# Kernel optimization log

Hardware: AMD Instinct MI355X
Metric: run time of the kernel (lower is better)

The kernel has to match this reference:

```python
import jax, jax.numpy as jnp
import numpy as np

B, T, D = 256, 256, 96   # batch, seq (== block_size), d_model
H, E = 6, 16             # n_head, d_head = d_model // n_head
DFF = 4 * D              # feedforward hidden = 384
NOISE_STD = 0.1
EPS = 1e-5               # torch LayerNorm default eps


def setup_inputs() -> dict:
    key = jax.random.key(0)
    ks = jax.random.split(key, 10)
    s = 0.02
    return {
        "x":     jax.random.normal(ks[0], (B, T, D), jnp.float32),
        # per-head Q/K/V projections stacked: [H, D, E] (no bias, as in Head)
        "Wq":    jax.random.normal(ks[1], (H, D, E), jnp.float32) * s,
        "Wk":    jax.random.normal(ks[2], (H, D, E), jnp.float32) * s,
        "Wv":    jax.random.normal(ks[3], (H, D, E), jnp.float32) * s,
        "Wp":    jax.random.normal(ks[4], (D, D), jnp.float32) * s,
        "bp":    jnp.zeros((D,), jnp.float32),
        "ln1_g": jnp.ones((D,), jnp.float32),
        "ln1_b": jnp.zeros((D,), jnp.float32),
        "ln2_g": jnp.ones((D,), jnp.float32),
        "ln2_b": jnp.zeros((D,), jnp.float32),
        "W1":    jax.random.normal(ks[5], (D, DFF), jnp.float32) * s,
        "b1":    jnp.zeros((DFF,), jnp.float32),
        "W2":    jax.random.normal(ks[6], (DFF, D), jnp.float32) * s,
        "b2":    jnp.zeros((D,), jnp.float32),
    }


def layernorm(x, g, b):
    m = jnp.mean(x, axis=-1, keepdims=True)
    v = jnp.var(x, axis=-1, keepdims=True)
    return (x - m) * jax.lax.rsqrt(v + EPS) * g + b


def reference(x, Wq, Wk, Wv, Wp, bp, ln1_g, ln1_b, ln2_g, ln2_b, W1, b1, W2, b2):
    Bx, Tx, Dx = x.shape
    nk1, nk2 = jax.random.split(jax.random.key(42), 2)

    # --- self-attention branch (pre-norm) ---
    h = layernorm(x, ln1_g, ln1_b)
    q = jnp.einsum('btd,hde->bhte', h, Wq)
    k = jnp.einsum('btd,hde->bhte', h, Wk)
    v = jnp.einsum('btd,hde->bhte', h, Wv)
    scores = jnp.einsum('bhte,bhse->bhts', q, k) * (E ** -0.5)
    causal = jnp.tril(jnp.ones((Tx, Tx), bool))
    scores = jnp.where(causal, scores, -jnp.inf)
    a = jax.nn.softmax(scores, axis=-1)      # dropout = identity (eval)
    o = jnp.einsum('bhts,bhse->bhte', a, v)
    o = o.transpose(0, 2, 1, 3).reshape(Bx, Tx, Dx)  # concat heads
    o = o @ Wp + bp
    x = x + o + jax.random.normal(nk1, x.shape, x.dtype) * NOISE_STD

    # --- feedforward branch (pre-norm) ---
    h = layernorm(x, ln2_g, ln2_b)
    f = jax.nn.relu(h @ W1 + b1) @ W2 + b2   # dropout = identity (eval)
    x = x + f + jax.random.normal(nk2, x.shape, x.dtype) * NOISE_STD
    return x
```

## Files before the change

kernel.cpp:

```cpp
#include <hip/hip_runtime.h>
#include <hip/hip_bf16.h>
#include <stdint.h>


#define B_    256
#define T_    256
#define D_    96
#define H_    6
#define E_    16
#define DFF_  384
#define BT_   (B_*T_)
#define NTOK_ (BT_*D_)
#define WPN_  (96*96)
#define W1N_  (96*384)
#define W2N_  (384*96)
#define WTOT_ (WPN_+W1N_+W2N_)

typedef __hip_bfloat16 bf16;
typedef __attribute__((ext_vector_type(8))) short v8s;
typedef __attribute__((ext_vector_type(4))) float v4f;

__device__ __forceinline__ void wfence(){ __asm__ volatile("" ::: "memory"); }

__host__ __device__ inline uint32_t rotl32(uint32_t x, int r){ return (x<<r)|(x>>(32-r)); }

__host__ __device__ inline void tf2x32(uint32_t k0, uint32_t k1, uint32_t& x0, uint32_t& x1){
  uint32_t ks2 = k0 ^ k1 ^ 0x1BD11BDAu;
  x0 += k0; x1 += k1;
#define TF_R(r) { x0 += x1; x1 = rotl32(x1, r); x1 ^= x0; }
  TF_R(13) TF_R(15) TF_R(26) TF_R(6)
  x0 += k1;  x1 += ks2 + 1u;
  TF_R(17) TF_R(29) TF_R(16) TF_R(24)
  x0 += ks2; x1 += k0 + 2u;
  TF_R(13) TF_R(15) TF_R(26) TF_R(6)
  x0 += k0;  x1 += k1 + 3u;
  TF_R(17) TF_R(29) TF_R(16) TF_R(24)
  x0 += k1;  x1 += ks2 + 4u;
  TF_R(13) TF_R(15) TF_R(26) TF_R(6)
  x0 += ks2; x1 += k0 + 5u;
#undef TF_R
}

__device__ __forceinline__ float erfinv32(float x){
  float w = -0.69314718056f * __log2f((1.0f - x) * (1.0f + x));
  float p;
  if (w < 5.0f) {
    w -= 2.5f;
    p = 2.81022636e-08f;
    p = fmaf(p, w, 3.43273939e-07f);
    p = fmaf(p, w, -3.5233877e-06f);
    p = fmaf(p, w, -4.39150654e-06f);
    p = fmaf(p, w, 0.00021858087f);
    p = fmaf(p, w, -0.00125372503f);
    p = fmaf(p, w, -0.00417768164f);
    p = fmaf(p, w, 0.246640727f);
    p = fmaf(p, w, 1.50140941f);
  } else {
    w = sqrtf(w) - 3.0f;
    p = -0.000200214257f;
    p = fmaf(p, w, 0.000100950558f);
    p = fmaf(p, w, 0.00134934322f);
    p = fmaf(p, w, -0.00367342844f);
    p = fmaf(p, w, 0.00573950773f);
    p = fmaf(p, w, -0.0076224613f);
    p = fmaf(p, w, 0.00943887047f);
    p = fmaf(p, w, 1.00167406f);
    p = fmaf(p, w, 2.83297682f);
  }
  return p * x;
}

__device__ __forceinline__ float jax_normal(uint32_t k0, uint32_t k1, uint32_t j){
  uint32_t x0 = 0u, x1 = j;
  tf2x32(k0, k1, x0, x1);
  uint32_t bits = x0 ^ x1;
  float f = __uint_as_float((bits >> 9) | 0x3F800000u) - 1.0f;
  const float lo = -0.99999994f;
  float u = fmaxf(lo, fmaf(f, 2.0f, lo));
  return 1.41421356f * erfinv32(u);
}

__device__ __forceinline__ float blo(uint32_t u){ return __uint_as_float(u << 16); }
__device__ __forceinline__ float bhi(uint32_t u){ return __uint_as_float(u & 0xFFFF0000u); }
__device__ __forceinline__ uint16_t f2b(float f){
  union { bf16 h; uint16_t u; } x; x.h = __float2bfloat16(f); return x.u;
}
__device__ __forceinline__ uint32_t packbf(float a, float b){
  return (uint32_t)f2b(a) | ((uint32_t)f2b(b) << 16);
}

__global__ __launch_bounds__(256, 3)
void k_attn_fused(const float* __restrict__ x,
                  const float* __restrict__ Wq, const float* __restrict__ Wk,
                  const float* __restrict__ Wv,
                  const float* __restrict__ g1, const float* __restrict__ bln1,
                  bf16* __restrict__ o_ws,
                  const float* __restrict__ Wp, const float* __restrict__ W1,
                  const float* __restrict__ W2, bf16* __restrict__ wbuf)
{
  __shared__ __align__(16) uint16_t hts[64*104];
  __shared__ __align__(16) uint32_t wpl[48][52];
  __shared__ __align__(16) uint16_t Ks[256][24];
  __shared__ __align__(16) uint16_t Vt[16][264];

  const int tid  = threadIdx.x;
  const int bh   = blockIdx.x;
  const int b    = bh / H_, h = bh % H_;
  const int w    = tid >> 6;
  const int lane = tid & 63;
  const int quad = lane >> 4;
  const int l15  = lane & 15;

  if (tid < 54) {
    int id = bh*54 + tid;
    const float* src; bf16* dst; int k, n, N;
    if (id < WPN_)             { src = Wp; dst = wbuf;               k = id/96; n = id%96; N = 96; }
    else if (id < WPN_ + W1N_) { int t = id - WPN_;
                                 src = W1; dst = wbuf + WPN_;        k = t/384; n = t%384; N = 384; }
    else                       { int t = id - WPN_ - W1N_;
                                 src = W2; dst = wbuf + WPN_ + W1N_; k = t/96;  n = t%96;  N = 96; }
    int idx = ((k>>3)*(N>>4) + (n>>4))*128 + ((n&15)<<3) + (k&7);
    dst[idx] = __float2bfloat16(src[(size_t)k*N + n]);
  }

  for (int idx = tid; idx < 48*48; idx += 256) {
    int c = idx / 48, dp = idx % 48;
    int mat = c >> 4, e = c & 15;
    const float* Wm = (mat == 0 ? Wk : (mat == 1 ? Wv : Wq)) + h*(D_*E_);
    wpl[c][dp] = packbf(Wm[(2*dp)*16 + e], Wm[(2*dp+1)*16 + e]);
  }

  v4f qacc[4];
  {
    const int r  = lane >> 2;
    const int cg = lane & 3;
    float gv[24], bv[24];
    #pragma unroll
    for (int i = 0; i < 24; ++i) { gv[i] = g1[cg*24 + i]; bv[i] = bln1[cg*24 + i]; }

    for (int rt = 0; rt < 4; ++rt) {
      __syncthreads();
      const int lrow = w*16 + r;
      const int row  = rt*64 + lrow;
      const float4* xp = (const float4*)(x + ((size_t)(b*256 + row)*96 + cg*24));
      float xv[24];
      #pragma unroll
      for (int p = 0; p < 6; ++p) {
        float4 t4 = xp[p];
        xv[4*p+0] = t4.x; xv[4*p+1] = t4.y; xv[4*p+2] = t4.z; xv[4*p+3] = t4.w;
      }
      float s1 = 0.f, s2 = 0.f;
      #pragma unroll
      for (int i = 0; i < 24; ++i) { s1 += xv[i]; s2 = fmaf(xv[i], xv[i], s2); }
      s1 += __shfl_xor(s1, 1); s2 += __shfl_xor(s2, 1);
      s1 += __shfl_xor(s1, 2); s2 += __shfl_xor(s2, 2);
      float mm = s1 * (1.0f/96.0f);
      float rs = rsqrtf(s2 * (1.0f/96.0f) - mm*mm + 1e-5f);
      #pragma unroll
      for (int p = 0; p < 12; ++p) {
        float h0 = (xv[2*p]   - mm)*rs*gv[2*p]   + bv[2*p];
        float h1 = (xv[2*p+1] - mm)*rs*gv[2*p+1] + bv[2*p+1];
        *(uint32_t*)&hts[lrow*104 + cg*24 + 2*p] = packbf(h0, h1);
      }
      __syncthreads();

      v8s ah[3];
      #pragma unroll
      for (int ks = 0; ks < 3; ++ks)
        ah[ks] = *(const v8s*)&hts[(w*16 + l15)*104 + ks*32 + quad*8];
      #pragma unroll
      for (int nt = 0; nt < 3; ++nt) {
        v4f acc = {0.f,0.f,0.f,0.f};
        #pragma unroll
        for (int ks = 0; ks < 3; ++ks) {
          v8s bb = *(const v8s*)&wpl[nt*16 + l15][ks*16 + quad*4];
          acc = __builtin_amdgcn_mfma_f32_16x16x32_bf16(ah[ks], bb, acc, 0, 0, 0);
        }
        int tr0 = rt*64 + w*16 + quad*4;
        if (nt == 0) {
          #pragma unroll
          for (int r2 = 0; r2 < 4; ++r2) Ks[tr0 + r2][l15] = f2b(acc[r2]);
        } else if (nt == 1) {
          *(uint32_t*)&Vt[l15][tr0]     = packbf(acc[0], acc[1]);
          *(uint32_t*)&Vt[l15][tr0 + 2] = packbf(acc[2], acc[3]);
        } else {
          qacc[rt] = acc;
        }
      }
    }
  }
  __syncthreads();

  uint16_t* Pb = &hts[(w*16)*104];
  v8s qf[4];
  v8s zero8;
  #pragma unroll
  for (int j = 0; j < 8; ++j) zero8[j] = 0;
  #pragma unroll
  for (int rt = 0; rt < 4; ++rt) {
    wfence();
    #pragma unroll
    for (int r2 = 0; r2 < 4; ++r2)
      Pb[(quad*4 + r2)*40 + l15] = f2b(qacc[rt][r2] * 0.25f);
    wfence();
    qf[rt] = (quad < 2) ? *(const v8s*)&Pb[l15*40 + quad*8] : zero8;
  }

  v8s ones;
  #pragma unroll
  for (int j = 0; j < 8; ++j) ones[j] = (short)0x3F80;

  v4f oacc[4], lac[4];
  #pragma unroll
  for (int i = 0; i < 4; ++i) { oacc[i] = (v4f){0.f,0.f,0.f,0.f}; lac[i] = (v4f){0.f,0.f,0.f,0.f}; }

  for (int sb = 0; sb < 8; ++sb) {
    v8s kf0 = (quad < 2) ? *(const v8s*)&Ks[sb*32      + l15][quad*8] : zero8;
    v8s kf1 = (quad < 2) ? *(const v8s*)&Ks[sb*32 + 16 + l15][quad*8] : zero8;
    v8s vf  = *(const v8s*)&Vt[l15][sb*32 + quad*8];
    #pragma unroll
    for (int i = 0; i < 4; ++i) {
      int mt = 4*i + w;
      if (mt >= 2*sb) {
        v4f z = {0.f,0.f,0.f,0.f};
        v4f s0 = __builtin_amdgcn_mfma_f32_16x16x32_bf16(qf[i], kf0, z, 0, 0, 0);
        v4f s1 = __builtin_amdgcn_mfma_f32_16x16x32_bf16(qf[i], kf1, z, 0, 0, 0);
        const int qb  = mt*16 + quad*4;
        const int sc0 = sb*32 + l15, sc1 = sc0 + 16;
        wfence();
        #pragma unroll
        for (int r2 = 0; r2 < 4; ++r2) {
          float p0 = (sc0 > qb + r2) ? 0.f : __expf(s0[r2]);
          float p1 = (sc1 > qb + r2) ? 0.f : __expf(s1[r2]);
          Pb[(quad*4 + r2)*40 + l15]      = f2b(p0);
          Pb[(quad*4 + r2)*40 + 16 + l15] = f2b(p1);
        }
        wfence();
        v8s pf = *(const v8s*)&Pb[l15*40 + quad*8];
        oacc[i] = __builtin_amdgcn_mfma_f32_16x16x32_bf16(pf, vf,   oacc[i], 0, 0, 0);
        lac[i]  = __builtin_amdgcn_mfma_f32_16x16x32_bf16(pf, ones, lac[i],  0, 0, 0);
      }
    }
  }

  #pragma unroll
  for (int i = 0; i < 4; ++i) {
    int mt = 4*i + w;
    #pragma unroll
    for (int r2 = 0; r2 < 4; ++r2) {
      float inv = 1.0f / lac[i][r2];
      size_t idx = ((size_t)b*256 + mt*16 + quad*4 + r2)*96 + h*16 + l15;
      o_ws[idx] = __float2bfloat16(oacc[i][r2] * inv);
    }
  }
}

__global__ __launch_bounds__(256, 6)
void k_proj_ff(const float* __restrict__ x, const bf16* __restrict__ o_ws,
               const bf16* __restrict__ wb,
               const float* __restrict__ bp,
               const float* __restrict__ g2, const float* __restrict__ bln2,
               const float* __restrict__ b1, const float* __restrict__ b2,
               float* __restrict__ out,
               uint32_t n1k0, uint32_t n1k1, uint32_t n2k0, uint32_t n2k1)
{
  __shared__ __align__(16) uint16_t t2[2][32][104];
  __shared__ __align__(8)  float2  st[32][2];

  const bf16* wpb = wb;
  const bf16* w1b = wb + WPN_;
  const bf16* w2b = wb + WPN_ + W1N_;

  const int tid  = threadIdx.x;
  const int w    = tid >> 6;
  const int wp   = w >> 1;
  const int s    = w & 1;
  const int lane = tid & 63;
  const int quad = lane >> 4;
  const int l15  = lane & 15;
  const int rowbase = blockIdx.x * 32;
  const uint32_t jbase = (uint32_t)rowbase * 96u;
  const int rloc = wp*16 + quad*4;

  #define BFRAG(Wb, Ndiv16, nt, k8) \
    (*(const v8s*)((Wb) + (((k8)*(Ndiv16) + (nt))*128 + l15*8)))

  float ff[12];
  {
    v8s ao[3];
    #pragma unroll
    for (int ks = 0; ks < 3; ++ks)
      ao[ks] = *(const v8s*)(o_ws + (size_t)(rowbase + wp*16 + l15)*96 + ks*32 + quad*8);
    #pragma unroll
    for (int nt3 = 0; nt3 < 3; ++nt3) {
      int nt = s*3 + nt3;
      int col = nt*16 + l15;
      v4f acc = {0.f,0.f,0.f,0.f};
      #pragma unroll
      for (int ks = 0; ks < 3; ++ks)
        acc = __builtin_amdgcn_mfma_f32_16x16x32_bf16(ao[ks], BFRAG(wpb, 6, nt, ks*4+quad), acc, 0, 0, 0);
      float bpv = bp[col];
      #pragma unroll
      for (int r = 0; r < 4; ++r) {
        int row = rloc + r;
        uint32_t j = jbase + (uint32_t)row*96u + (uint32_t)col;
        ff[nt3*4+r] = acc[r] + bpv + x[j] + 0.1f * jax_normal(n1k0, n1k1, j);
      }
    }
  }

  {
    float s1p[4], s2p[4];
    #pragma unroll
    for (int r = 0; r < 4; ++r) {
      float s1 = 0.f, s2 = 0.f;
      #pragma unroll
      for (int nt3 = 0; nt3 < 3; ++nt3) { float v = ff[nt3*4+r]; s1 += v; s2 = fmaf(v, v, s2); }
      s1 += __shfl_xor(s1, 1); s2 += __shfl_xor(s2, 1);
      s1 += __shfl_xor(s1, 2); s2 += __shfl_xor(s2, 2);
      s1 += __shfl_xor(s1, 4); s2 += __shfl_xor(s2, 4);
      s1 += __shfl_xor(s1, 8); s2 += __shfl_xor(s2, 8);
      s1p[r] = s1; s2p[r] = s2;
    }
    if (l15 == 0) {
      #pragma unroll
      for (int r = 0; r < 4; ++r) st[rloc + r][s] = make_float2(s1p[r], s2p[r]);
    }
    __syncthreads();

    float g2v[3], b2l[3];
    #pragma unroll
    for (int nt3 = 0; nt3 < 3; ++nt3) {
      g2v[nt3] = g2[s*48 + nt3*16 + l15];
      b2l[nt3] = bln2[s*48 + nt3*16 + l15];
    }
    #pragma unroll
    for (int r = 0; r < 4; ++r) {
      float2 pa = st[rloc + r][0], pb = st[rloc + r][1];
      float s1 = pa.x + pb.x, s2 = pa.y + pb.y;
      float mm = s1 * (1.0f/96.0f);
      float rs = rsqrtf(s2 * (1.0f/96.0f) - mm*mm + 1e-5f);
      #pragma unroll
      for (int nt3 = 0; nt3 < 3; ++nt3)
        t2[0][rloc + r][s*48 + nt3*16 + l15] =
            f2b((ff[nt3*4+r] - mm) * rs * g2v[nt3] + b2l[nt3]);
    }
  }
  __syncthreads();

  v8s ah[3];
  #pragma unroll
  for (int ks = 0; ks < 3; ++ks)
    ah[ks] = *(const v8s*)&t2[0][wp*16 + l15][ks*32 + quad*8];
  v4f acc2[3];
  #pragma unroll
  for (int nt3 = 0; nt3 < 3; ++nt3) acc2[nt3] = (v4f){0.f,0.f,0.f,0.f};
  float n2v[12];

  #define FF1C(C, DST) { \
    _Pragma("unroll") \
    for (int nt3 = 0; nt3 < 3; ++nt3) { \
      v4f a = {0.f,0.f,0.f,0.f}; \
      _Pragma("unroll") \
      for (int ks = 0; ks < 3; ++ks) \
        a = __builtin_amdgcn_mfma_f32_16x16x32_bf16(ah[ks], BFRAG(w1b, 24, (C)*6 + s*3 + nt3, ks*4+quad), a, 0, 0, 0); \
      float b1v = b1[(C)*96 + s*48 + nt3*16 + l15]; \
      _Pragma("unroll") \
      for (int r = 0; r < 4; ++r) \
        DST[rloc + r][s*48 + nt3*16 + l15] = f2b(fmaxf(a[r] + b1v, 0.f)); \
    } }

  #define FF2C(C, SRC) { \
    v8s af[3]; \
    _Pragma("unroll") \
    for (int ks = 0; ks < 3; ++ks) \
      af[ks] = *(const v8s*)&SRC[wp*16 + l15][ks*32 + quad*8]; \
    _Pragma("unroll") \
    for (int nt3 = 0; nt3 < 3; ++nt3) { \
      _Pragma("unroll") \
      for (int ks = 0; ks < 3; ++ks) \
        acc2[nt3] = __builtin_amdgcn_mfma_f32_16x16x32_bf16(af[ks], BFRAG(w2b, 6, s*3 + nt3, ((C)*3+ks)*4+quad), acc2[nt3], 0, 0, 0); \
    } }

  #define GEN3(C) { \
    _Pragma("unroll") \
    for (int i = 0; i < 3; ++i) { \
      int vv = (C)*3 + i; int nt2 = vv >> 2; int r2 = vv & 3; \
      int row = rloc + r2; \
      uint32_t j = jbase + (uint32_t)row*96u + (uint32_t)(s*48 + nt2*16 + l15); \
      n2v[vv] = jax_normal(n2k0, n2k1, j); \
    } }

  FF1C(0, t2[1])
  __syncthreads();
  FF1C(1, t2[0])
  FF2C(0, t2[1])
  GEN3(0)
  __syncthreads();
  FF1C(2, t2[1])
  FF2C(1, t2[0])
  GEN3(1)
  __syncthreads();
  FF1C(3, t2[0])
  FF2C(2, t2[1])
  GEN3(2)
  __syncthreads();
  FF2C(3, t2[0])
  GEN3(3)

  #pragma unroll
  for (int nt3 = 0; nt3 < 3; ++nt3) {
    int col = s*48 + nt3*16 + l15;
    float b2v = b2[col];
    #pragma unroll
    for (int r = 0; r < 4; ++r) {
      int row = rloc + r;
      out[(size_t)(rowbase + row)*96 + col] =
          ff[nt3*4+r] + acc2[nt3][r] + b2v + 0.1f * n2v[nt3*4 + r];
    }
  }
  #undef GEN3
  #undef FF2C
  #undef FF1C
  #undef BFRAG
}

__global__ __launch_bounds__(256)
void k_zero(float* __restrict__ out)
{
  int i = blockIdx.x*256 + threadIdx.x;
  if (i < NTOK_) out[i] = 0.0f;
}

extern "C" void kernel_launch(void* const* d_in, const int* in_sizes, int n_in,
                              void* d_out, int out_size, void* d_ws, size_t ws_size,
                              hipStream_t stream) {
  const float* x    = (const float*)d_in[0];
  const float* Wq   = (const float*)d_in[1];
  const float* Wk   = (const float*)d_in[2];
  const float* Wv   = (const float*)d_in[3];
  const float* Wp   = (const float*)d_in[4];
  const float* bp   = (const float*)d_in[5];
  const float* g1   = (const float*)d_in[6];
  const float* bln1 = (const float*)d_in[7];
  const float* g2   = (const float*)d_in[8];
  const float* bln2 = (const float*)d_in[9];
  const float* W1   = (const float*)d_in[10];
  const float* b1   = (const float*)d_in[11];
  const float* W2   = (const float*)d_in[12];
  const float* b2   = (const float*)d_in[13];
  float* out = (float*)d_out;

  size_t need = (size_t)NTOK_*sizeof(bf16) + (size_t)WTOT_*sizeof(bf16);
  if (ws_size < need) {
    hipLaunchKernelGGL(k_zero, dim3((NTOK_ + 255)/256), dim3(256), 0, stream, out);
    return;
  }
  bf16* o_ws = (bf16*)d_ws;
  bf16* wbuf = o_ws + NTOK_;

  uint32_t n1k0 = 0u, n1k1 = 0u; tf2x32(0u, 42u, n1k0, n1k1);
  uint32_t n2k0 = 0u, n2k1 = 1u; tf2x32(0u, 42u, n2k0, n2k1);

  hipLaunchKernelGGL(k_attn_fused, dim3(B_*H_), dim3(256), 0, stream,
                     x, Wq, Wk, Wv, g1, bln1, o_ws, Wp, W1, W2, wbuf);
  hipLaunchKernelGGL(k_proj_ff, dim3(BT_/32), dim3(256), 0, stream,
                     x, o_ws, wbuf, bp, g2, bln2, b1, b2, out,
                     n1k0, n1k1, n2k0, n2k1);
}
```

Baseline: 197.1 us.

## Split LayerNorm1 into separate kernel writing bf16 activations to output buffer

LayerNorm1 moves out of the attention kernel into a standalone kernel that writes bf16 normalized rows into the output buffer, used as scratch. Before the split, each of the 6 head blocks per batch recomputed the same LayerNorm. The attention kernel now loads MFMA A-fragments straight from global memory, which frees shared memory and lets launch bounds rise from 3 to 4 blocks per CU. The cost is an extra kernel launch plus a global round-trip for the bf16 activations.

```diff
diff --git a/kernel.cpp b/kernel.cpp
--- a/kernel.cpp
+++ b/kernel.cpp
@@ -89,16 +89,55 @@
   return (uint32_t)f2b(a) | ((uint32_t)f2b(b) << 16);
 }
 
-__global__ __launch_bounds__(256, 3)
-void k_attn_fused(const float* __restrict__ x,
+__global__ __launch_bounds__(256, 8)
+void k_ln1(const float* __restrict__ x,
+           const float* __restrict__ g1, const float* __restrict__ bln1,
+           bf16* __restrict__ h1)
+{
+  const int tid  = threadIdx.x;
+  const int wv   = tid >> 6;
+  const int lane = tid & 63;
+  const int r    = lane >> 2;
+  const int cg   = lane & 3;
+  const int row  = blockIdx.x*64 + wv*16 + r;
+
+  float gv[24], bv[24];
+  #pragma unroll
+  for (int i = 0; i < 24; ++i) { gv[i] = g1[cg*24 + i]; bv[i] = bln1[cg*24 + i]; }
+
+  const float4* xp = (const float4*)(x + (size_t)row*96 + cg*24);
+  float xv[24];
+  #pragma unroll
+  for (int p = 0; p < 6; ++p) {
+    float4 t4 = xp[p];
+    xv[4*p+0] = t4.x; xv[4*p+1] = t4.y; xv[4*p+2] = t4.z; xv[4*p+3] = t4.w;
+  }
+  float s1 = 0.f, s2 = 0.f;
+  #pragma unroll
+  for (int i = 0; i < 24; ++i) { s1 += xv[i]; s2 = fmaf(xv[i], xv[i], s2); }
+  s1 += __shfl_xor(s1, 1); s2 += __shfl_xor(s2, 1);
+  s1 += __shfl_xor(s1, 2); s2 += __shfl_xor(s2, 2);
+  float mm = s1 * (1.0f/96.0f);
+  float rs = rsqrtf(s2 * (1.0f/96.0f) - mm*mm + 1e-5f);
+
+  uint32_t* hw = (uint32_t*)h1 + (size_t)row*48 + cg*12;
+  #pragma unroll
+  for (int p = 0; p < 12; ++p) {
+    float h0 = (xv[2*p]   - mm)*rs*gv[2*p]   + bv[2*p];
+    float h1v= (xv[2*p+1] - mm)*rs*gv[2*p+1] + bv[2*p+1];
+    hw[p] = packbf(h0, h1v);
+  }
+}
+
+__global__ __launch_bounds__(256, 4)
+void k_attn_fused(const bf16* __restrict__ h1,
                   const float* __restrict__ Wq, const float* __restrict__ Wk,
                   const float* __restrict__ Wv,
-                  const float* __restrict__ g1, const float* __restrict__ bln1,
                   bf16* __restrict__ o_ws,
                   const float* __restrict__ Wp, const float* __restrict__ W1,
                   const float* __restrict__ W2, bf16* __restrict__ wbuf)
 {
-  __shared__ __align__(16) uint16_t hts[64*104];
+  __shared__ __align__(16) uint16_t Pbuf[4][640];
   __shared__ __align__(16) uint32_t wpl[48][52];
   __shared__ __align__(16) uint16_t Ks[256][24];
   __shared__ __align__(16) uint16_t Vt[16][264];
@@ -129,69 +168,39 @@
     const float* Wm = (mat == 0 ? Wk : (mat == 1 ? Wv : Wq)) + h*(D_*E_);
     wpl[c][dp] = packbf(Wm[(2*dp)*16 + e], Wm[(2*dp+1)*16 + e]);
   }
+  __syncthreads();
 
   v4f qacc[4];
-  {
-    const int r  = lane >> 2;
-    const int cg = lane & 3;
-    float gv[24], bv[24];
-    #pragma unroll
-    for (int i = 0; i < 24; ++i) { gv[i] = g1[cg*24 + i]; bv[i] = bln1[cg*24 + i]; }
-
-    for (int rt = 0; rt < 4; ++rt) {
-      __syncthreads();
-      const int lrow = w*16 + r;
-      const int row  = rt*64 + lrow;
-      const float4* xp = (const float4*)(x + ((size_t)(b*256 + row)*96 + cg*24));
-      float xv[24];
-      #pragma unroll
-      for (int p = 0; p < 6; ++p) {
-        float4 t4 = xp[p];
-        xv[4*p+0] = t4.x; xv[4*p+1] = t4.y; xv[4*p+2] = t4.z; xv[4*p+3] = t4.w;
+  #pragma unroll
+  for (int rt = 0; rt < 4; ++rt) {
+    const size_t grow = (size_t)(b*256 + rt*64 + w*16 + l15)*96;
+    v8s ah[3];
+    #pragma unroll
+    for (int ks = 0; ks < 3; ++ks)
+      ah[ks] = *(const v8s*)(h1 + grow + ks*32 + quad*8);
+    #pragma unroll
+    for (int nt = 0; nt < 3; ++nt) {
+      v4f acc = {0.f,0.f,0.f,0.f};
+      #pragma unroll
+      for (int ks = 0; ks < 3; ++ks) {
+        v8s bb = *(const v8s*)&wpl[nt*16 + l15][ks*16 + quad*4];
+        acc = __builtin_amdgcn_mfma_f32_16x16x32_bf16(ah[ks], bb, acc, 0, 0, 0);
       }
-      float s1 = 0.f, s2 = 0.f;
-      #pragma unroll
-      for (int i = 0; i < 24; ++i) { s1 += xv[i]; s2 = fmaf(xv[i], xv[i], s2); }
-      s1 += __shfl_xor(s1, 1); s2 += __shfl_xor(s2, 1);
-      s1 += __shfl_xor(s1, 2); s2 += __shfl_xor(s2, 2);
-      float mm = s1 * (1.0f/96.0f);
-      float rs = rsqrtf(s2 * (1.0f/96.0f) - mm*mm + 1e-5f);
-      #pragma unroll
-      for (int p = 0; p < 12; ++p) {
-        float h0 = (xv[2*p]   - mm)*rs*gv[2*p]   + bv[2*p];
-        float h1 = (xv[2*p+1] - mm)*rs*gv[2*p+1] + bv[2*p+1];
-        *(uint32_t*)&hts[lrow*104 + cg*24 + 2*p] = packbf(h0, h1);
+      int tr0 = rt*64 + w*16 + quad*4;
+      if (nt == 0) {
+        #pragma unroll
+        for (int r2 = 0; r2 < 4; ++r2) Ks[tr0 + r2][l15] = f2b(acc[r2]);
+      } else if (nt == 1) {
+        *(uint32_t*)&Vt[l15][tr0]     = packbf(acc[0], acc[1]);
+        *(uint32_t*)&Vt[l15][tr0 + 2] = packbf(acc[2], acc[3]);
+      } else {
+        qacc[rt] = acc;
       }
-      __syncthreads();
-
-      v8s ah[3];
-      #pragma unroll
-      for (int ks = 0; ks < 3; ++ks)
-        ah[ks] = *(const v8s*)&hts[(w*16 + l15)*104 + ks*32 + quad*8];
-      #pragma unroll
-      for (int nt = 0; nt < 3; ++nt) {
-        v4f acc = {0.f,0.f,0.f,0.f};
-        #pragma unroll
-        for (int ks = 0; ks < 3; ++ks) {
-          v8s bb = *(const v8s*)&wpl[nt*16 + l15][ks*16 + quad*4];
-          acc = __builtin_amdgcn_mfma_f32_16x16x32_bf16(ah[ks], bb, acc, 0, 0, 0);
-        }
-        int tr0 = rt*64 + w*16 + quad*4;
-        if (nt == 0) {
-          #pragma unroll
-          for (int r2 = 0; r2 < 4; ++r2) Ks[tr0 + r2][l15] = f2b(acc[r2]);
-        } else if (nt == 1) {
-          *(uint32_t*)&Vt[l15][tr0]     = packbf(acc[0], acc[1]);
-          *(uint32_t*)&Vt[l15][tr0 + 2] = packbf(acc[2], acc[3]);
-        } else {
-          qacc[rt] = acc;
-        }
-      }
-    }
-  }
-  __syncthreads();
-
-  uint16_t* Pb = &hts[(w*16)*104];
+    }
+  }
+  __syncthreads();
+
+  uint16_t* Pb = &Pbuf[w][0];
   v8s qf[4];
   v8s zero8;
   #pragma unroll
@@ -458,12 +467,15 @@
   }
   bf16* o_ws = (bf16*)d_ws;
   bf16* wbuf = o_ws + NTOK_;
+  bf16* h1   = (bf16*)d_out;
 
   uint32_t n1k0 = 0u, n1k1 = 0u; tf2x32(0u, 42u, n1k0, n1k1);
   uint32_t n2k0 = 0u, n2k1 = 1u; tf2x32(0u, 42u, n2k0, n2k1);
 
+  hipLaunchKernelGGL(k_ln1, dim3(BT_/64), dim3(256), 0, stream,
+                     x, g1, bln1, h1);
   hipLaunchKernelGGL(k_attn_fused, dim3(B_*H_), dim3(256), 0, stream,
-                     x, Wq, Wk, Wv, g1, bln1, o_ws, Wp, W1, W2, wbuf);
+                     h1, Wq, Wk, Wv, o_ws, Wp, W1, W2, wbuf);
   hipLaunchKernelGGL(k_proj_ff, dim3(BT_/32), dim3(256), 0, stream,
                      x, o_ws, wbuf, bp, g2, bln2, b1, b2, out,
                      n1k0, n1k1, n2k0, n2k1);
```

Result: no change. 200.6 us (+1.8%).

## Software-pipeline attention P tiles with a double-buffered LDS staging area

Applied to the files above, without the earlier changes.

Restructures the per-key-block inner loop so the exp/P write for query tile I is interleaved with the PV and row-sum MFMAs for tile I-1. The P staging buffer alternates between two 640-element halves, and the last tile is drained after the loop. The aim is to hide LDS write-to-read latency and keep MFMA units busy instead of serializing write-fence-read for each tile. This needs twice the LDS for the P buffer; the declaration is not visible here, so the buffer may need enlarging. It also raises register pressure.

```diff
diff --git a/kernel.cpp b/kernel.cpp
--- a/kernel.cpp
+++ b/kernel.cpp
@@ -218,28 +218,40 @@
     v8s kf0 = (quad < 2) ? *(const v8s*)&Ks[sb*32      + l15][quad*8] : zero8;
     v8s kf1 = (quad < 2) ? *(const v8s*)&Ks[sb*32 + 16 + l15][quad*8] : zero8;
     v8s vf  = *(const v8s*)&Vt[l15][sb*32 + quad*8];
-    #pragma unroll
-    for (int i = 0; i < 4; ++i) {
-      int mt = 4*i + w;
-      if (mt >= 2*sb) {
-        v4f z = {0.f,0.f,0.f,0.f};
-        v4f s0 = __builtin_amdgcn_mfma_f32_16x16x32_bf16(qf[i], kf0, z, 0, 0, 0);
-        v4f s1 = __builtin_amdgcn_mfma_f32_16x16x32_bf16(qf[i], kf1, z, 0, 0, 0);
-        const int qb  = mt*16 + quad*4;
-        const int sc0 = sb*32 + l15, sc1 = sc0 + 16;
-        wfence();
-        #pragma unroll
-        for (int r2 = 0; r2 < 4; ++r2) {
-          float p0 = (sc0 > qb + r2) ? 0.f : __expf(s0[r2]);
-          float p1 = (sc1 > qb + r2) ? 0.f : __expf(s1[r2]);
-          Pb[(quad*4 + r2)*40 + l15]      = f2b(p0);
-          Pb[(quad*4 + r2)*40 + 16 + l15] = f2b(p1);
-        }
-        wfence();
-        v8s pf = *(const v8s*)&Pb[l15*40 + quad*8];
-        oacc[i] = __builtin_amdgcn_mfma_f32_16x16x32_bf16(pf, vf,   oacc[i], 0, 0, 0);
-        lac[i]  = __builtin_amdgcn_mfma_f32_16x16x32_bf16(pf, ones, lac[i],  0, 0, 0);
-      }
+    const int sc0 = sb*32 + l15, sc1 = sc0 + 16;
+
+    #define STG(I) { \
+      if (4*(I)+w >= 2*sb) { \
+        v4f z = {0.f,0.f,0.f,0.f}; \
+        v4f s0 = __builtin_amdgcn_mfma_f32_16x16x32_bf16(qf[(I)], kf0, z, 0, 0, 0); \
+        v4f s1 = __builtin_amdgcn_mfma_f32_16x16x32_bf16(qf[(I)], kf1, z, 0, 0, 0); \
+        const int qb = (4*(I)+w)*16 + quad*4; \
+        wfence();    \
+        uint16_t* bw = Pb + (((I)&1)*640); \
+        _Pragma("unroll") \
+        for (int r2 = 0; r2 < 4; ++r2) { \
+          float p0 = (sc0 > qb + r2) ? 0.f : __expf(s0[r2]); \
+          float p1 = (sc1 > qb + r2) ? 0.f : __expf(s1[r2]); \
+          bw[(quad*4 + r2)*40 + l15]      = f2b(p0); \
+          bw[(quad*4 + r2)*40 + 16 + l15] = f2b(p1); \
+        } \
+      } \
+      if ((I) > 0 && (4*((I)-1)+w >= 2*sb)) { \
+        const uint16_t* br = Pb + ((((I)-1)&1)*640); \
+        v8s pf = *(const v8s*)&br[l15*40 + quad*8]; \
+        oacc[(I)-1] = __builtin_amdgcn_mfma_f32_16x16x32_bf16(pf, vf,   oacc[(I)-1], 0, 0, 0); \
+        lac[(I)-1]  = __builtin_amdgcn_mfma_f32_16x16x32_bf16(pf, ones, lac[(I)-1],  0, 0, 0); \
+      } }
+
+    STG(0) STG(1) STG(2) STG(3)
+    #undef STG
+
+    if (12 + w >= 2*sb) {
+      wfence();
+      const uint16_t* br = Pb + 640;
+      v8s pf = *(const v8s*)&br[l15*40 + quad*8];
+      oacc[3] = __builtin_amdgcn_mfma_f32_16x16x32_bf16(pf, vf,   oacc[3], 0, 0, 0);
+      lac[3]  = __builtin_amdgcn_mfma_f32_16x16x32_bf16(pf, ones, lac[3],  0, 0, 0);
     }
   }
 
```

New measurement: 198.4 us. Within noise of the previous version (+0.7%).
